# Kernel tuning notes

Measured on AMD Instinct MI355X. Metric: run time of the kernel, lower is better.

Reference implementation:

```python
import jax, jax.numpy as jnp
import numpy as np
import math

T, B, V, D = 8, 32, 50257, 256
N = 4096            # memory slots
H = 4               # attention heads
L = 2               # transformer layers
K = 3               # shift width
HALF = K // 2
WIN = 16            # controller window
RH, WH = 1, 1       # read / write heads
EPS = 1e-12


def _pe(win, d):
    pos = jnp.arange(win, dtype=jnp.float32)[:, None]
    div = jnp.exp(jnp.arange(0, d, 2, dtype=jnp.float32) * (-math.log(10000.0) / d))
    pe = jnp.zeros((win, d), dtype=jnp.float32)
    pe = pe.at[:, 0::2].set(jnp.sin(pos * div))
    pe = pe.at[:, 1::2].set(jnp.cos(pos * div))
    return pe[:, None, :]


def _ln(x, g, b, eps=1e-5):
    mu = x.mean(-1, keepdims=True)
    var = ((x - mu) ** 2).mean(-1, keepdims=True)
    return (x - mu) * jax.lax.rsqrt(var + eps) * g + b


def _mha(x, Wqkv, bqkv, Wo, bo):
    S, Bc, Dm = x.shape
    dh = Dm // H
    qkv = x @ Wqkv.T + bqkv
    q, k, v = jnp.split(qkv, 3, axis=-1)
    q = q.reshape(S, Bc, H, dh)
    k = k.reshape(S, Bc, H, dh)
    v = v.reshape(S, Bc, H, dh)
    logits = jnp.einsum('sbhd,tbhd->bhst', q, k) / math.sqrt(dh)
    a = jax.nn.softmax(logits, axis=-1)
    o = jnp.einsum('bhst,tbhd->sbhd', a, v).reshape(S, Bc, Dm)
    return o @ Wo.T + bo


def _addressing(key_v, beta, gate, shift, gamma, prev_w, memory):
    # key_v [B,M], beta/gate/gamma [B,1], shift [B,K], prev_w [B,N], memory [B,N,M]
    key_n = key_v / (jnp.linalg.norm(key_v, axis=-1, keepdims=True) + EPS)
    mem_n = memory / (jnp.linalg.norm(memory, axis=-1, keepdims=True) + EPS)
    cos = jnp.einsum('bnm,bm->bn', mem_n, key_n)
    wc = jax.nn.softmax(jax.nn.softplus(beta) * cos, axis=-1)
    g = jax.nn.sigmoid(gate)
    wg = g * wc + (1.0 - g) * prev_w
    s = jax.nn.softmax(shift, axis=-1)
    shifted = sum(s[:, k:k + 1] * jnp.roll(wg, k - HALF, axis=-1) for k in range(K))
    gp = 1.0 + jax.nn.softplus(gamma)
    wt = (shifted + EPS) ** gp
    return wt / (wt.sum(-1, keepdims=True) + EPS)


def setup_inputs() -> dict:
    key = jax.random.key(0)
    ks = iter(jax.random.split(key, 40))
    def w(shape, s=0.02):
        return jax.random.normal(next(ks), shape, jnp.float32) * s
    return {
        'tokens': jax.random.randint(next(ks), (T, B), 0, V, jnp.int32),
        'emb_W': w((V, D)),
        'read_gate_W': w((D, D)), 'read_gate_b': jnp.zeros((D,)),
        'film_W': w((2 * D, D)), 'film_b': jnp.zeros((2 * D,)),
        't_Wqkv': w((L, 3 * D, D)), 't_bqkv': jnp.zeros((L, 3 * D)),
        't_Wo': w((L, D, D)), 't_bo': jnp.zeros((L, D)),
        't_ln1_g': jnp.ones((L, D)), 't_ln1_b': jnp.zeros((L, D)),
        't_ln2_g': jnp.ones((L, D)), 't_ln2_b': jnp.zeros((L, D)),
        't_W1': w((L, 4 * D, D)), 't_b1': jnp.zeros((L, 4 * D)),
        't_W2': w((L, D, 4 * D)), 't_b2': jnp.zeros((L, D)),
        'out_ln_g': jnp.ones((D,)), 'out_ln_b': jnp.zeros((D,)),
        'lstm_Wih': w((2, 4 * D, D)), 'lstm_Whh': w((2, 4 * D, D)),
        'lstm_bih': jnp.zeros((2, 4 * D)), 'lstm_bhh': jnp.zeros((2, 4 * D)),
        'head_W': w((V, D)), 'head_b': jnp.zeros((V,)),
        'read_W': w((D + 3 + K, D)), 'read_b': jnp.zeros((D + 3 + K,)),
        'write_W': w((3 * D + 3 + K, D)), 'write_b': jnp.zeros((3 * D + 3 + K,)),
    }


def reference(tokens, emb_W, read_gate_W, read_gate_b, film_W, film_b,
              t_Wqkv, t_bqkv, t_Wo, t_bo, t_ln1_g, t_ln1_b, t_ln2_g, t_ln2_b,
              t_W1, t_b1, t_W2, t_b2, out_ln_g, out_ln_b,
              lstm_Wih, lstm_Whh, lstm_bih, lstm_bhh,
              head_W, head_b, read_W, read_b, write_W, write_b):
    pe = _pe(WIN, D)
    memory = jnp.zeros((B, N, D), jnp.float32)
    read_w = jnp.zeros((B, RH, N), jnp.float32).at[:, :, 0].set(1.0)
    write_w = jnp.zeros((B, WH, N), jnp.float32).at[:, :, 0].set(1.0)
    record = jnp.zeros((B, D), jnp.float32)
    hx = jnp.zeros((2, B, D), jnp.float32)
    cx = jnp.zeros((2, B, D), jnp.float32)
    hist = jnp.zeros((1, B, D), jnp.float32)
    logits_all = []
    for t in range(T):  # T fixed, sequential recurrence (context length grows)
        emb = emb_W[tokens[t]]                               # [B,D]
        r = jnp.einsum('bhn,bnm->bm', read_w, memory)        # sum over read heads
        fp = record @ film_W.T + film_b
        gam = 1.0 + jnp.tanh(fp[:, :D])
        bet = fp[:, D:]
        rg = jax.nn.sigmoid(record @ read_gate_W.T + read_gate_b)
        x_in = gam * emb + bet + rg * r
        ctx = jnp.concatenate([hist, x_in[None]], axis=0)
        if ctx.shape[0] > WIN:
            ctx = ctx[-WIN:]
        hist = ctx
        h = ctx + pe[:ctx.shape[0]]
        for l in range(L):  # norm_first pre-LN encoder layers (eval, relu FFN)
            h = h + _mha(_ln(h, t_ln1_g[l], t_ln1_b[l]), t_Wqkv[l], t_bqkv[l], t_Wo[l], t_bo[l])
            h = h + (jax.nn.relu(_ln(h, t_ln2_g[l], t_ln2_b[l]) @ t_W1[l].T + t_b1[l]) @ t_W2[l].T + t_b2[l])
        c_out = _ln(h[-1], out_ln_g, out_ln_b)
        # 2-layer LSTM single step (torch gate order i,f,g,o)
        x_l = c_out
        new_h, new_c = [], []
        for l in range(2):
            gates = x_l @ lstm_Wih[l].T + lstm_bih[l] + hx[l] @ lstm_Whh[l].T + lstm_bhh[l]
            i_g, f_g, g_g, o_g = jnp.split(gates, 4, axis=-1)
            c_new = jax.nn.sigmoid(f_g) * cx[l] + jax.nn.sigmoid(i_g) * jnp.tanh(g_g)
            h_new = jax.nn.sigmoid(o_g) * jnp.tanh(c_new)
            new_h.append(h_new); new_c.append(c_new)
            x_l = h_new
        hx = jnp.stack(new_h); cx = jnp.stack(new_c)
        record = hx[-1]
        c_out = c_out + x_l
        logits_all.append(c_out @ head_W.T + head_b)
        # read addressing
        rp = (c_out @ read_W.T + read_b).reshape(B, RH, -1)
        new_rw = []
        for hh in range(RH):
            p = rp[:, hh]
            new_rw.append(_addressing(p[:, :D], p[:, D:D + 1], p[:, D + 1:D + 2],
                                      p[:, D + 2:D + 2 + K], p[:, D + 2 + K:D + 3 + K],
                                      read_w[:, hh], memory))
        read_w = jnp.stack(new_rw, axis=1)
        # write addressing + erase/add (addressing uses pre-update memory)
        wp = (c_out @ write_W.T + write_b).reshape(B, WH, -1)
        mem_pre = memory
        new_ww = []
        for hh in range(WH):
            p = wp[:, hh]
            wt = _addressing(p[:, :D], p[:, D:D + 1], p[:, D + 1:D + 2],
                             p[:, D + 2:D + 2 + K], p[:, D + 2 + K:D + 3 + K],
                             write_w[:, hh], mem_pre)
            erase = jax.nn.sigmoid(p[:, D + 3 + K:2 * D + 3 + K])
            add = jnp.tanh(p[:, 2 * D + 3 + K:3 * D + 3 + K])
            memory = memory * (1.0 - wt[:, :, None] * erase[:, None, :]) + wt[:, :, None] * add[:, None, :]
            new_ww.append(wt)
        write_w = jnp.stack(new_ww, axis=1)
    return jnp.stack(logits_all, axis=0)  # [T, B, V]
```

## Files before the change

### kernel.cpp

```cpp
#include <hip/hip_runtime.h>
#include <math.h>

#define TT 8
#define BB 32
#define VV 50257
#define DD 256
#define NN 4096
#define EPS_ 1e-12f

typedef __attribute__((ext_vector_type(8))) short short8;
typedef __attribute__((ext_vector_type(4))) float f32x4;

__device__ __forceinline__ float sigf(float x) { return 1.f / (1.f + expf(-x)); }
__device__ __forceinline__ float softplusf_(float x) { return fmaxf(x, 0.f) + log1pf(expf(-fabsf(x))); }
__device__ __forceinline__ unsigned f2bf(float f) {
  union { float f; unsigned u; } c; c.f = f;
  return (c.u + 0x7FFFu + ((c.u >> 16) & 1u)) >> 16;
}
__device__ __forceinline__ float bf2f(unsigned u16) {
  union { unsigned u; float f; } c; c.u = u16 << 16; return c.f;
}

__device__ __forceinline__ float blk_sum(float v, float* s) {
#pragma unroll
  for (int o = 32; o > 0; o >>= 1) v += __shfl_down(v, o);
  __syncthreads();
  if ((threadIdx.x & 63) == 0) s[threadIdx.x >> 6] = v;
  __syncthreads();
  return s[0] + s[1] + s[2] + s[3];
}
__device__ __forceinline__ float blk_max(float v, float* s) {
#pragma unroll
  for (int o = 32; o > 0; o >>= 1) v = fmaxf(v, __shfl_down(v, o));
  __syncthreads();
  if ((threadIdx.x & 63) == 0) s[threadIdx.x >> 6] = v;
  __syncthreads();
  return fmaxf(fmaxf(s[0], s[1]), fmaxf(s[2], s[3]));
}

__global__ void init_k(float* rw, float* ww, float* hpe) {
  int i = blockIdx.x * 256 + threadIdx.x;
  if (i < BB) { rw[(size_t)i * NN] = 1.f; ww[(size_t)i * NN] = 1.f; }
  if (i < BB * DD) hpe[i] = (i & 1) ? 1.f : 0.f;
}

__global__ void cvtw_k(const float* __restrict__ W, unsigned short* __restrict__ Wh, int n4) {
  int i = blockIdx.x * 256 + threadIdx.x;
  if (i >= n4) return;
  float4 v = *(const float4*)(W + (size_t)i * 4);
  uint2 p;
  p.x = f2bf(v.x) | (f2bf(v.y) << 16);
  p.y = f2bf(v.z) | (f2bf(v.w) << 16);
  *(uint2*)(Wh + (size_t)i * 4) = p;
}

__global__ void catlstm_k(const float* __restrict__ Wih, const float* __restrict__ Whh,
                          const float* __restrict__ bih, const float* __restrict__ bhh,
                          unsigned short* __restrict__ Wc, float* __restrict__ cb) {
  int i = blockIdx.x * 256 + threadIdx.x;
  if (i >= 2 * 1024 * 512) return;
  int k = i & 511, np = (i >> 9) & 1023, l = i >> 19;
  int d = np >> 2, gate = np & 3;
  int src = gate * 256 + d;
  float v = (k < 256) ? Wih[((size_t)l * 1024 + src) * 256 + k]
                      : Whh[((size_t)l * 1024 + src) * 256 + (k - 256)];
  Wc[i] = (unsigned short)f2bf(v);
  if (k == 0) cb[l * 1024 + np] = bih[l * 1024 + src] + bhh[l * 1024 + src];
}

__global__ void catrw_k(const float* __restrict__ rW, const float* __restrict__ rb,
                        const float* __restrict__ wW, const float* __restrict__ wb,
                        unsigned short* __restrict__ Wrw, float* __restrict__ brw) {
  int i = blockIdx.x * 256 + threadIdx.x;
  if (i >= 1036 * 256) return;
  int k = i & 255, n = i >> 8;
  float v = (n < 262) ? rW[(size_t)n * 256 + k] : wW[(size_t)(n - 262) * 256 + k];
  Wrw[i] = (unsigned short)f2bf(v);
  if (k == 0) brw[n] = (n < 262) ? rb[n] : wb[n - 262];
}

__global__ void brc_k(const float* __restrict__ fb, const float* __restrict__ rb, float* __restrict__ brc) {
  int i = blockIdx.x * 256 + threadIdx.x;
  if (i < 512) brc[i] = fb[i];
  else if (i < 768) brc[i] = rb[i - 512];
}

__global__ __launch_bounds__(256) void ln0_k(const float* __restrict__ hpe,
                                             const float* __restrict__ g1, const float* __restrict__ b1,
                                             unsigned short* __restrict__ q1b) {
  __shared__ float s8[8];
  int b = blockIdx.x, d = threadIdx.x;
  float v = hpe[(size_t)b * 256 + d];
  float mu = blk_sum(v, s8) * (1.f / 256.f);
  float dd = v - mu;
  float var = blk_sum(dd * dd, s8) * (1.f / 256.f);
  float rs = rsqrtf(var + 1e-5f);
  q1b[(size_t)b * 256 + d] = (unsigned short)f2bf(dd * rs * g1[d] + b1[d]);
}

__device__ __forceinline__ void gA32f_dev(const unsigned short* __restrict__ A,
                                          const unsigned short* __restrict__ W,
                                          const float* __restrict__ bias,
                                          float* __restrict__ Cf, int ldc, int Nlim, int nblk) {
  const int tid = threadIdx.x, w = tid >> 6, l = tid & 63, r = l & 15, q = l >> 4;
  const int n = nblk * 64 + w * 16 + r;
  const unsigned short* Wp = W + (size_t)n * 256;
  f32x4 acc0 = {0.f, 0.f, 0.f, 0.f}, acc1 = {0.f, 0.f, 0.f, 0.f};
#pragma unroll
  for (int kt = 0; kt < 8; ++kt) {
    short8 a0 = *(const short8*)(A + r * 256 + kt * 32 + q * 8);
    short8 a1 = *(const short8*)(A + (16 + r) * 256 + kt * 32 + q * 8);
    short8 bf = *(const short8*)(Wp + kt * 32 + q * 8);
    acc0 = __builtin_amdgcn_mfma_f32_16x16x32_bf16(a0, bf, acc0, 0, 0, 0);
    acc1 = __builtin_amdgcn_mfma_f32_16x16x32_bf16(a1, bf, acc1, 0, 0, 0);
  }
  if (n >= Nlim) return;
  float bb = bias[n];
#pragma unroll
  for (int e = 0; e < 4; ++e) {
    int m1 = q * 4 + e, m2 = m1 + 16;
    Cf[(size_t)m1 * ldc + n] = acc0[e] + bb;
    Cf[(size_t)m2 * ldc + n] = acc1[e] + bb;
  }
}

__global__ __launch_bounds__(256) void gA_k(const unsigned short* __restrict__ A,
                                            const unsigned short* __restrict__ W,
                                            const float* __restrict__ bias,
                                            float* __restrict__ Cf, int ldc, int Nlim) {
  gA32f_dev(A + (size_t)blockIdx.y * 32 * 256, W, bias,
            Cf + (size_t)blockIdx.y * 32 * ldc, ldc, Nlim, blockIdx.x);
}

__global__ __launch_bounds__(256) void gAr_k(const unsigned short* __restrict__ A,
                                             const unsigned short* __restrict__ W,
                                             const float* __restrict__ bias,
                                             unsigned short* __restrict__ Cb, int ldc) {
  const int tid = threadIdx.x, w = tid >> 6, l = tid & 63, r = l & 15, q = l >> 4;
  const int n = blockIdx.x * 64 + w * 16 + r;
  const unsigned short* Ap = A + (size_t)blockIdx.y * 32 * 256;
  unsigned short* Cp = Cb + (size_t)blockIdx.y * 32 * ldc;
  const unsigned short* Wp = W + (size_t)n * 256;
  f32x4 acc0 = {0.f, 0.f, 0.f, 0.f}, acc1 = {0.f, 0.f, 0.f, 0.f};
#pragma unroll
  for (int kt = 0; kt < 8; ++kt) {
    short8 a0 = *(const short8*)(Ap + r * 256 + kt * 32 + q * 8);
    short8 a1 = *(const short8*)(Ap + (16 + r) * 256 + kt * 32 + q * 8);
    short8 bf = *(const short8*)(Wp + kt * 32 + q * 8);
    acc0 = __builtin_amdgcn_mfma_f32_16x16x32_bf16(a0, bf, acc0, 0, 0, 0);
    acc1 = __builtin_amdgcn_mfma_f32_16x16x32_bf16(a1, bf, acc1, 0, 0, 0);
  }
  float bb = bias[n];
#pragma unroll
  for (int e = 0; e < 4; ++e) {
    int m1 = q * 4 + e, m2 = m1 + 16;
    Cb[(size_t)(blockIdx.y * 32 + m1) * ldc + n] = (unsigned short)f2bf(fmaxf(acc0[e] + bb, 0.f));
    Cb[(size_t)(blockIdx.y * 32 + m2) * ldc + n] = (unsigned short)f2bf(fmaxf(acc1[e] + bb, 0.f));
  }
  (void)Cp;
}

template <int K>
__global__ __launch_bounds__(256) void gC_k(const unsigned short* __restrict__ A,
                                            const unsigned short* __restrict__ W,
                                            const float* __restrict__ bias,
                                            const float* __restrict__ resid,
                                            float* __restrict__ Hout) {
  const int tid = threadIdx.x, w = tid >> 6, l = tid & 63, r = l & 15, q = l >> 4;
  const int n = blockIdx.x * 64 + w * 16 + r;
  const int m0 = blockIdx.y * 32;
  const unsigned short* Ap = A + (size_t)m0 * K;
  const unsigned short* Wp = W + (size_t)n * K;
  f32x4 acc0 = {0.f, 0.f, 0.f, 0.f}, acc1 = {0.f, 0.f, 0.f, 0.f};
#pragma unroll 4
  for (int kt = 0; kt < K / 32; ++kt) {
    short8 a0 = *(const short8*)(Ap + (size_t)r * K + kt * 32 + q * 8);
    short8 a1 = *(const short8*)(Ap + (size_t)(16 + r) * K + kt * 32 + q * 8);
    short8 bf = *(const short8*)(Wp + kt * 32 + q * 8);
    acc0 = __builtin_amdgcn_mfma_f32_16x16x32_bf16(a0, bf, acc0, 0, 0, 0);
    acc1 = __builtin_amdgcn_mfma_f32_16x16x32_bf16(a1, bf, acc1, 0, 0, 0);
  }
  float bb = bias[n];
#pragma unroll
  for (int e = 0; e < 4; ++e) {
    int m1 = m0 + q * 4 + e, m2 = m1 + 16;
    Hout[(size_t)m1 * 256 + n] = acc0[e] + bb + resid[(size_t)m1 * 256 + n];
    Hout[(size_t)m2 * 256 + n] = acc1[e] + bb + resid[(size_t)m2 * 256 + n];
  }
}

__global__ __launch_bounds__(256) void addLN_k(const float* __restrict__ H,
                                               const float* __restrict__ g,
                                               const float* __restrict__ be,
                                               unsigned short* __restrict__ Xb, int xstride,
                                               float* __restrict__ c_out) {
  const int tid = threadIdx.x, w = tid >> 6, l = tid & 63;
  const int m0 = blockIdx.x * 32;
  const float4 g4 = *(const float4*)(g + l * 4);
  const float4 b4 = *(const float4*)(be + l * 4);
#pragma unroll
  for (int i = 0; i < 8; ++i) {
    int row = m0 + w * 8 + i;
    float4 v = *(const float4*)(H + (size_t)row * 256 + l * 4);
    float s1 = v.x + v.y + v.z + v.w;
    float s2 = v.x * v.x + v.y * v.y + v.z * v.z + v.w * v.w;
#pragma unroll
    for (int o = 32; o > 0; o >>= 1) { s1 += __shfl_xor(s1, o); s2 += __shfl_xor(s2, o); }
    float mu = s1 * (1.f / 256.f);
    float var = fmaxf(s2 * (1.f / 256.f) - mu * mu, 0.f);
    float rs = rsqrtf(var + 1e-5f);
    float y0 = (v.x - mu) * rs * g4.x + b4.x;
    float y1 = (v.y - mu) * rs * g4.y + b4.y;
    float y2 = (v.z - mu) * rs * g4.z + b4.z;
    float y3 = (v.w - mu) * rs * g4.w + b4.w;
    uint2 pk;
    pk.x = f2bf(y0) | (f2bf(y1) << 16);
    pk.y = f2bf(y2) | (f2bf(y3) << 16);
    *(uint2*)(Xb + (size_t)row * xstride + l * 4) = pk;
    if (c_out) {
      float4 cv = make_float4(y0, y1, y2, y3);
      *(float4*)(c_out + (size_t)row * 256 + l * 4) = cv;
    }
  }
}

__global__ __launch_bounds__(256) void auxg_k(const unsigned short* __restrict__ cfinb,
                                              const unsigned short* __restrict__ Wrw,
                                              const float* __restrict__ brw, float* __restrict__ rpwp,
                                              const unsigned short* __restrict__ record_b,
                                              const unsigned short* __restrict__ FRw,
                                              const float* __restrict__ brc, float* __restrict__ fp) {
  if (blockIdx.x < 17) gA32f_dev(cfinb, Wrw, brw, rpwp, 1036, 1036, blockIdx.x);
  else gA32f_dev(record_b, FRw, brc, fp, 768, 768, blockIdx.x - 17);
}

__global__ __launch_bounds__(128) void attn_k(const float* __restrict__ qkv,
                                              unsigned short* __restrict__ ao, int S) {
  int bh = blockIdx.x;
  int b = bh >> 2, h = bh & 3;
  __shared__ float q[9][64], k[9][64], v[9][64], lg[9][12];
  int tid = threadIdx.x;
  for (int i = tid; i < S * 64; i += 128) {
    int s = i >> 6, d = i & 63;
    const float* base = qkv + (size_t)(s * BB + b) * 768 + h * 64 + d;
    q[s][d] = base[0]; k[s][d] = base[256]; v[s][d] = base[512];
  }
  __syncthreads();
  for (int p = tid; p < S * S; p += 128) {
    int s = p / S, t2 = p % S;
    float acc = 0.f;
    for (int d = 0; d < 64; ++d) acc += q[s][d] * k[t2][d];
    lg[s][t2] = acc * 0.125f;
  }
  __syncthreads();
  if (tid < S) {
    float mx = -1e30f;
    for (int t2 = 0; t2 < S; ++t2) mx = fmaxf(mx, lg[tid][t2]);
    float sum = 0.f;
    for (int t2 = 0; t2 < S; ++t2) { float e = expf(lg[tid][t2] - mx); lg[tid][t2] = e; sum += e; }
    float inv = 1.f / sum;
    for (int t2 = 0; t2 < S; ++t2) lg[tid][t2] *= inv;
  }
  __syncthreads();
  for (int i = tid; i < S * 64; i += 128) {
    int s = i >> 6, d = i & 63;
    float o = 0.f;
    for (int t2 = 0; t2 < S; ++t2) o += lg[s][t2] * v[t2][d];
    ao[(size_t)(s * BB + b) * 256 + h * 64 + d] = (unsigned short)f2bf(o);
  }
}

__global__ __launch_bounds__(64) void attnl_k(const float* __restrict__ qkv,
                                              unsigned short* __restrict__ ao, int S) {
  int bh = blockIdx.x;
  int b = bh >> 2, h = bh & 3;
  int d = threadIdx.x;
  __shared__ float sc[9];
  float qd = qkv[(size_t)((S - 1) * BB + b) * 768 + h * 64 + d];
  for (int j = 0; j < S; ++j) {
    float p = qd * qkv[(size_t)(j * BB + b) * 768 + h * 64 + 256 + d];
#pragma unroll
    for (int o = 32; o > 0; o >>= 1) p += __shfl_down(p, o);
    if (d == 0) sc[j] = p * 0.125f;
  }
  __syncthreads();
  float mx = -1e30f;
  for (int j = 0; j < S; ++j) mx = fmaxf(mx, sc[j]);
  float pj[9], sum = 0.f;
  for (int j = 0; j < S; ++j) { pj[j] = expf(sc[j] - mx); sum += pj[j]; }
  float inv = 1.f / sum;
  float o = 0.f;
  for (int j = 0; j < S; ++j) o += pj[j] * inv * qkv[(size_t)(j * BB + b) * 768 + h * 64 + 512 + d];
  ao[(size_t)b * 256 + h * 64 + d] = (unsigned short)f2bf(o);
}

template <int LAST>
__global__ __launch_bounds__(256) void gL_k(const unsigned short* __restrict__ A,
                                            const unsigned short* __restrict__ W,
                                            const float* __restrict__ cbias,
                                            float* __restrict__ cx,
                                            unsigned short* __restrict__ li_own,
                                            unsigned short* __restrict__ li_next,
                                            const float* __restrict__ c_outp,
                                            unsigned short* __restrict__ cfinb,
                                            unsigned short* __restrict__ record_b) {
  __shared__ float g[32][68];
  const int tid = threadIdx.x, w = tid >> 6, l = tid & 63, r = l & 15, q = l >> 4;
  const int n = blockIdx.x * 64 + w * 16 + r;
  const unsigned short* Wp = W + (size_t)n * 512;
  f32x4 acc0 = {0.f, 0.f, 0.f, 0.f}, acc1 = {0.f, 0.f, 0.f, 0.f};
#pragma unroll 4
  for (int kt = 0; kt < 16; ++kt) {
    short8 a0 = *(const short8*)(A + (size_t)r * 512 + kt * 32 + q * 8);
    short8 a1 = *(const short8*)(A + (size_t)(16 + r) * 512 + kt * 32 + q * 8);
    short8 bf = *(const short8*)(Wp + kt * 32 + q * 8);
    acc0 = __builtin_amdgcn_mfma_f32_16x16x32_bf16(a0, bf, acc0, 0, 0, 0);
    acc1 = __builtin_amdgcn_mfma_f32_16x16x32_bf16(a1, bf, acc1, 0, 0, 0);
  }
  float bb = cbias[n];
  int nb = w * 16 + r;
#pragma unroll
  for (int e = 0; e < 4; ++e) {
    g[q * 4 + e][nb] = acc0[e] + bb;
    g[16 + q * 4 + e][nb] = acc1[e] + bb;
  }
  __syncthreads();
#pragma unroll
  for (int h2 = 0; h2 < 2; ++h2) {
    int u = tid + 256 * h2;
    int b = u >> 4, dd = u & 15;
    int dg = blockIdx.x * 16 + dd;
    float gi = g[b][dd * 4 + 0], gf = g[b][dd * 4 + 1];
    float gg = g[b][dd * 4 + 2], go = g[b][dd * 4 + 3];
    float c = sigf(gf) * cx[b * 256 + dg] + sigf(gi) * tanhf(gg);
    float hN = sigf(go) * tanhf(c);
    cx[b * 256 + dg] = c;
    li_own[(size_t)b * 512 + 256 + dg] = (unsigned short)f2bf(hN);
    if constexpr (LAST) {
      record_b[b * 256 + dg] = (unsigned short)f2bf(hN);
      cfinb[b * 256 + dg] = (unsigned short)f2bf(c_outp[b * 256 + dg] + hN);
    } else {
      li_next[(size_t)b * 512 + dg] = (unsigned short)f2bf(hN);
    }
  }
}

__global__ __launch_bounds__(256) void xinpw_k(const int* __restrict__ tokens,
                                               const float* __restrict__ embW,
                                               const float* __restrict__ fp,
                                               const float* __restrict__ rvec,
                                               const float* __restrict__ g1, const float* __restrict__ b1,
                                               float* __restrict__ hpe,
                                               unsigned short* __restrict__ q1b, int t) {
  __shared__ float s8[8];
  int b = blockIdx.x, d = threadIdx.x;
  float gam = 1.f + tanhf(fp[(size_t)b * 768 + d]);
  float bet = fp[(size_t)b * 768 + 256 + d];
  float rg = sigf(fp[(size_t)b * 768 + 512 + d]);
  int tok = tokens[t * BB + b];
  float emb = embW[(size_t)tok * 256 + d];
  float ang = (float)(t + 1) * expf(-logf(10000.f) * (float)(d & ~1) / 256.f);
  float pe = (d & 1) ? cosf(ang) : sinf(ang);
  float x = gam * emb + bet + rg * rvec[b * 256 + d] + pe;
  hpe[((size_t)(t + 1) * BB + b) * 256 + d] = x;
  float mu = blk_sum(x, s8) * (1.f / 256.f);
  float dd = x - mu;
  float var = blk_sum(dd * dd, s8) * (1.f / 256.f);
  float rs = rsqrtf(var + 1e-5f);
  q1b[((size_t)(t + 1) * BB + b) * 256 + d] = (unsigned short)f2bf(dd * rs * g1[d] + b1[d]);
}

__global__ __launch_bounds__(256) void fusePA_k(const unsigned short* __restrict__ Wh,
                                                const unsigned short* __restrict__ Ah,
                                                const float* __restrict__ hb,
                                                float* __restrict__ out,
                                                const unsigned short* __restrict__ mem,
                                                const float* __restrict__ rpwp,
                                                float* __restrict__ dr,
                                                float* __restrict__ dw,
                                                float* __restrict__ nrm) {
  __shared__ float kr[256], kw[256];
  const int bid = blockIdx.x;
  const int tid = threadIdx.x;
  if (bid < 786) {
    const int w = tid >> 6, l = tid & 63;
    const int r = l & 15, q = l >> 4;
    const int n = bid * 64 + w * 16 + r;
    const int nc = n < VV ? n : VV - 1;
    const short* Ap = (const short*)Ah;
    const short* Wp = (const short*)Wh + (size_t)nc * 256;
    short8 a0[8], a1[8], bf[8];
#pragma unroll
    for (int kt = 0; kt < 8; ++kt) {
      a0[kt] = *(const short8*)(Ap + r * 256 + kt * 32 + q * 8);
      a1[kt] = *(const short8*)(Ap + (16 + r) * 256 + kt * 32 + q * 8);
      bf[kt] = *(const short8*)(Wp + kt * 32 + q * 8);
    }
    f32x4 acc0 = {0.f, 0.f, 0.f, 0.f}, acc1 = {0.f, 0.f, 0.f, 0.f};
#pragma unroll
    for (int kt = 0; kt < 8; ++kt) {
      acc0 = __builtin_amdgcn_mfma_f32_16x16x32_bf16(a0[kt], bf[kt], acc0, 0, 0, 0);
      acc1 = __builtin_amdgcn_mfma_f32_16x16x32_bf16(a1[kt], bf[kt], acc1, 0, 0, 0);
    }
    if (n < VV) {
      float bb = hb[n];
#pragma unroll
      for (int e = 0; e < 4; ++e) {
        int m = q * 4 + e;
        out[(size_t)m * VV + n] = acc0[e] + bb;
        out[(size_t)(16 + m) * VV + n] = acc1[e] + bb;
      }
    }
    return;
  }
  const int idx = bid - 786;
  const int bx = idx & 255, by = idx >> 8;
  kr[tid] = rpwp[(size_t)by * 1036 + tid];
  kw[tid] = rpwp[(size_t)by * 1036 + 262 + tid];
  __syncthreads();
  int w = tid >> 6, lane = tid & 63;
  float4 kr4 = *(float4*)&kr[lane * 4];
  float4 kw4 = *(float4*)&kw[lane * 4];
  int n0 = bx * 16 + w * 4;
  for (int rr = 0; rr < 4; ++rr) {
    int n = n0 + rr;
    const unsigned short* row = mem + ((size_t)by * NN + n) * 256;
    uint2 pck = *(const uint2*)(row + lane * 4);
    float m0 = bf2f(pck.x & 0xffffu), m1 = bf2f(pck.x >> 16);
    float m2 = bf2f(pck.y & 0xffffu), m3 = bf2f(pck.y >> 16);
    float pr = m0 * kr4.x + m1 * kr4.y + m2 * kr4.z + m3 * kr4.w;
    float pw = m0 * kw4.x + m1 * kw4.y + m2 * kw4.z + m3 * kw4.w;
    float pn = m0 * m0 + m1 * m1 + m2 * m2 + m3 * m3;
#pragma unroll
    for (int o = 32; o > 0; o >>= 1) {
      pr += __shfl_down(pr, o); pw += __shfl_down(pw, o); pn += __shfl_down(pn, o);
    }
    if (lane == 0) {
      dr[(size_t)by * NN + n] = pr;
      dw[(size_t)by * NN + n] = pw;
      nrm[(size_t)by * NN + n] = pn;
    }
  }
}

__global__ __launch_bounds__(256) void addr_k(const float* __restrict__ dr,
                                              const float* __restrict__ dw,
                                              const float* __restrict__ nrm,
                                              const float* __restrict__ rpwp,
                                              float* rw, float* ww,
                                              float* __restrict__ ea,
                                              float* __restrict__ rvec) {
  __shared__ float wg[4096];
  __shared__ float s8[8];
  int head = blockIdx.x & 1, b = blockIdx.x >> 1;
  int tid = threadIdx.x;
  const float* p = rpwp + (size_t)b * 1036 + (head ? 262 : 0);
  const float* dot = (head ? dw : dr) + (size_t)b * NN;
  const float* n2 = nrm + (size_t)b * NN;
  float* wout = (head ? ww : rw) + (size_t)b * NN;

  float kv = p[tid];
  float kn = sqrtf(blk_sum(kv * kv, s8)) + EPS_;
  float beta = p[256], gate = p[257], sh0 = p[258], sh1 = p[259], sh2 = p[260], gamma = p[261];
  float spb = softplusf_(beta);
  float g = sigf(gate);
  float mx3 = fmaxf(sh0, fmaxf(sh1, sh2));
  float e0 = expf(sh0 - mx3), e1 = expf(sh1 - mx3), e2 = expf(sh2 - mx3);
  float esum = e0 + e1 + e2;
  float s0 = e0 / esum, s1 = e1 / esum, s2 = e2 / esum;
  float gp = 1.f + softplusf_(gamma);

  float l[16];
  float lmax = -1e30f;
#pragma unroll
  for (int i = 0; i < 16; ++i) {
    int n = tid + i * 256;
    float cs = dot[n] / ((sqrtf(n2[n]) + EPS_) * kn);
    l[i] = spb * cs;
    lmax = fmaxf(lmax, l[i]);
  }
  float Mx = blk_max(lmax, s8);
  float es = 0.f;
#pragma unroll
  for (int i = 0; i < 16; ++i) { l[i] = expf(l[i] - Mx); es += l[i]; }
  float SS = blk_sum(es, s8);
  float inv = 1.f / SS;
#pragma unroll
  for (int i = 0; i < 16; ++i) {
    int n = tid + i * 256;
    wg[n] = g * l[i] * inv + (1.f - g) * wout[n];
  }
  __syncthreads();
  float wt[16];
  float wsum = 0.f;
#pragma unroll
  for (int i = 0; i < 16; ++i) {
    int n = tid + i * 256;
    float sh = s0 * wg[(n + 1) & 4095] + s1 * wg[n] + s2 * wg[(n + 4095) & 4095];
    wt[i] = powf(sh + EPS_, gp);
    wsum += wt[i];
  }
  float WS = blk_sum(wsum, s8) + EPS_;
  float winv = 1.f / WS;
#pragma unroll
  for (int i = 0; i < 16; ++i) wout[tid + i * 256] = wt[i] * winv;

  if (head) {
    ea[(size_t)b * 512 + tid] = sigf(p[262 + tid]);
    ea[(size_t)b * 512 + 256 + tid] = tanhf(p[518 + tid]);
  } else {
    rvec[(size_t)b * 256 + tid] = 0.f;
  }
}

template <int FIRST>
__global__ __launch_bounds__(256) void passB_k(unsigned short* mem, const float* __restrict__ ww,
                                               const float* __restrict__ rw,
                                               const float* __restrict__ ea,
                                               float* __restrict__ rvec) {
  __shared__ float eS[256], aS[256];
  __shared__ float rred[4][256];
  int b = blockIdx.y, tid = threadIdx.x;
  eS[tid] = ea[(size_t)b * 512 + tid];
  aS[tid] = ea[(size_t)b * 512 + 256 + tid];
  __syncthreads();
  int w = tid >> 6, lane = tid & 63;
  float4 e4 = *(float4*)&eS[lane * 4];
  float4 a4 = *(float4*)&aS[lane * 4];
  float4 racc = make_float4(0.f, 0.f, 0.f, 0.f);
  int n0 = blockIdx.x * 128 + w * 32;
  for (int rr = 0; rr < 32; ++rr) {
    int n = n0 + rr;
    float wt = ww[(size_t)b * NN + n];
    float rwv = rw[(size_t)b * NN + n];
    unsigned short* row = mem + ((size_t)b * NN + n) * 256;
    float m0, m1, m2, m3;
    if (FIRST) {
      m0 = wt * a4.x; m1 = wt * a4.y; m2 = wt * a4.z; m3 = wt * a4.w;
    } else {
      uint2 p = *(const uint2*)(row + lane * 4);
      m0 = bf2f(p.x & 0xffffu) * (1.f - wt * e4.x) + wt * a4.x;
      m1 = bf2f(p.x >> 16) * (1.f - wt * e4.y) + wt * a4.y;
      m2 = bf2f(p.y & 0xffffu) * (1.f - wt * e4.z) + wt * a4.z;
      m3 = bf2f(p.y >> 16) * (1.f - wt * e4.w) + wt * a4.w;
    }
    uint2 pk;
    pk.x = f2bf(m0) | (f2bf(m1) << 16);
    pk.y = f2bf(m2) | (f2bf(m3) << 16);
    *(uint2*)(row + lane * 4) = pk;
    racc.x += rwv * m0; racc.y += rwv * m1; racc.z += rwv * m2; racc.w += rwv * m3;
  }
  rred[w][lane * 4 + 0] = racc.x;
  rred[w][lane * 4 + 1] = racc.y;
  rred[w][lane * 4 + 2] = racc.z;
  rred[w][lane * 4 + 3] = racc.w;
  __syncthreads();
  float s = rred[0][tid] + rred[1][tid] + rred[2][tid] + rred[3][tid];
  atomicAdd(rvec + (size_t)b * 256 + tid, s);
}

extern "C" void kernel_launch(void* const* d_in, const int* in_sizes, int n_in,
                              void* d_out, int out_size, void* d_ws, size_t ws_size,
                              hipStream_t stream) {
  const int* tokens = (const int*)d_in[0];
  const float* emb_W = (const float*)d_in[1];
  const float* read_gate_W = (const float*)d_in[2];
  const float* read_gate_b = (const float*)d_in[3];
  const float* film_W = (const float*)d_in[4];
  const float* film_b = (const float*)d_in[5];
  const float* t_Wqkv = (const float*)d_in[6];
  const float* t_bqkv = (const float*)d_in[7];
  const float* t_Wo = (const float*)d_in[8];
  const float* t_bo = (const float*)d_in[9];
  const float* t_ln1_g = (const float*)d_in[10];
  const float* t_ln1_b = (const float*)d_in[11];
  const float* t_ln2_g = (const float*)d_in[12];
  const float* t_ln2_b = (const float*)d_in[13];
  const float* t_W1 = (const float*)d_in[14];
  const float* t_b1 = (const float*)d_in[15];
  const float* t_W2 = (const float*)d_in[16];
  const float* t_b2 = (const float*)d_in[17];
  const float* out_ln_g = (const float*)d_in[18];
  const float* out_ln_b = (const float*)d_in[19];
  const float* lstm_Wih = (const float*)d_in[20];
  const float* lstm_Whh = (const float*)d_in[21];
  const float* lstm_bih = (const float*)d_in[22];
  const float* lstm_bhh = (const float*)d_in[23];
  const float* head_W = (const float*)d_in[24];
  const float* head_b = (const float*)d_in[25];
  const float* read_W = (const float*)d_in[26];
  const float* read_b = (const float*)d_in[27];
  const float* write_W = (const float*)d_in[28];
  const float* write_b = (const float*)d_in[29];
  float* out = (float*)d_out;

  float* ws = (float*)d_ws;
  size_t off = 0;
  float* read_w = ws + off; off += (size_t)BB * NN;
  float* write_w = ws + off; off += (size_t)BB * NN;
  float* cx = ws + off; off += 2 * BB * DD;
  float* r_vec = ws + off; off += BB * DD;
  float* dot_r = ws + off; off += (size_t)BB * NN;
  float* dot_w = ws + off; off += (size_t)BB * NN;
  float* norm2 = ws + off; off += (size_t)BB * NN;
  unsigned short* record_b = (unsigned short*)(ws + off); off += BB * DD / 2;
  unsigned short* lstm_in_b = (unsigned short*)(ws + off); off += 2 * BB * 512 / 2;
  size_t zero_floats = off;
  unsigned short* memory = (unsigned short*)(ws + off); off += (size_t)BB * NN * DD / 2;
  float* hpe = ws + off; off += 9 * BB * DD;
  float* h = ws + off; off += 9 * BB * DD;
  float* h2 = ws + off; off += BB * DD;
  float* qkvC = ws + off; off += 9 * BB * 768;
  float* qkv2 = ws + off; off += 9 * BB * 768;
  float* fp = ws + off; off += BB * 768;
  float* c_out = ws + off; off += BB * DD;
  float* rpwp = ws + off; off += BB * 1036;
  float* ea = ws + off; off += BB * 2 * DD;
  unsigned short* q1b = (unsigned short*)(ws + off); off += 9 * BB * DD / 2;
  unsigned short* q2b = (unsigned short*)(ws + off); off += 9 * BB * DD / 2;
  unsigned short* x2b = (unsigned short*)(ws + off); off += 9 * BB * DD / 2;
  unsigned short* x2b2 = (unsigned short*)(ws + off); off += BB * DD / 2;
  unsigned short* ao1_b = (unsigned short*)(ws + off); off += 9 * BB * DD / 2;
  unsigned short* ao2_b = (unsigned short*)(ws + off); off += BB * DD / 2;
  unsigned short* mid_b = (unsigned short*)(ws + off); off += 9 * BB * 1024 / 2;
  unsigned short* cfinb = (unsigned short*)(ws + off); off += BB * DD / 2;
  unsigned short* Wh = (unsigned short*)(ws + off); off += (size_t)VV * 256 / 2;
  unsigned short* Wq_b = (unsigned short*)(ws + off); off += 2 * 768 * 256 / 2;
  unsigned short* Wo_b = (unsigned short*)(ws + off); off += 2 * 256 * 256 / 2;
  unsigned short* W1_b = (unsigned short*)(ws + off); off += 2 * 1024 * 256 / 2;
  unsigned short* W2_b = (unsigned short*)(ws + off); off += 2 * 256 * 1024 / 2;
  unsigned short* Wc_b = (unsigned short*)(ws + off); off += 2 * 1024 * 512 / 2;
  unsigned short* Wrw_b = (unsigned short*)(ws + off); off += 1088 * 256 / 2;
  unsigned short* FR_b = (unsigned short*)(ws + off); off += 768 * 256 / 2;
  float* cb2 = ws + off; off += 2 * 1024;
  float* brw = ws + off; off += 1040;
  float* brc = ws + off; off += 768;
  if (ws_size < off * sizeof(float)) return;

  (void)hipMemsetAsync(ws, 0, zero_floats * sizeof(float), stream);
  (void)hipMemsetAsync(Wrw_b + (size_t)1036 * 256, 0, (size_t)52 * 256 * 2, stream);
  init_k<<<32, 256, 0, stream>>>(read_w, write_w, hpe);
  cvtw_k<<<(VV * 256 / 4 + 255) / 256, 256, 0, stream>>>(head_W, Wh, VV * 256 / 4);
  cvtw_k<<<(2 * 768 * 256 / 4 + 255) / 256, 256, 0, stream>>>(t_Wqkv, Wq_b, 2 * 768 * 256 / 4);
  cvtw_k<<<(2 * 256 * 256 / 4 + 255) / 256, 256, 0, stream>>>(t_Wo, Wo_b, 2 * 256 * 256 / 4);
  cvtw_k<<<(2 * 1024 * 256 / 4 + 255) / 256, 256, 0, stream>>>(t_W1, W1_b, 2 * 1024 * 256 / 4);
  cvtw_k<<<(2 * 256 * 1024 / 4 + 255) / 256, 256, 0, stream>>>(t_W2, W2_b, 2 * 256 * 1024 / 4);
  cvtw_k<<<(512 * 256 / 4 + 255) / 256, 256, 0, stream>>>(film_W, FR_b, 512 * 256 / 4);
  cvtw_k<<<(256 * 256 / 4 + 255) / 256, 256, 0, stream>>>(read_gate_W, FR_b + 512 * 256, 256 * 256 / 4);
  catlstm_k<<<4096, 256, 0, stream>>>(lstm_Wih, lstm_Whh, lstm_bih, lstm_bhh, Wc_b, cb2);
  catrw_k<<<1036, 256, 0, stream>>>(read_W, read_b, write_W, write_b, Wrw_b, brw);
  brc_k<<<3, 256, 0, stream>>>(film_b, read_gate_b, brc);
  ln0_k<<<BB, 256, 0, stream>>>(hpe, t_ln1_g, t_ln1_b, q1b);
  gA_k<<<dim3(12, 1), 256, 0, stream>>>(q1b, Wq_b, t_bqkv, qkvC, 768, 768);
  gA_k<<<dim3(12, 1), 256, 0, stream>>>(record_b, FR_b, brc, fp, 768, 768);

  for (int t = 0; t < TT; ++t) {
    const int S = t + 2;

    xinpw_k<<<BB, 256, 0, stream>>>(tokens, emb_W, fp, r_vec, t_ln1_g, t_ln1_b, hpe, q1b, t);
    gA_k<<<dim3(12, 1), 256, 0, stream>>>(q1b + (size_t)(t + 1) * BB * 256, Wq_b, t_bqkv,
                                          qkvC + (size_t)(t + 1) * BB * 768, 768, 768);
    attn_k<<<BB * 4, 128, 0, stream>>>(qkvC, ao1_b, S);
    gC_k<256><<<dim3(4, S), 256, 0, stream>>>(ao1_b, Wo_b, t_bo, hpe, h);
    addLN_k<<<S, 256, 0, stream>>>(h, t_ln2_g, t_ln2_b, x2b, 256, nullptr);
    gAr_k<<<dim3(16, S), 256, 0, stream>>>(x2b, W1_b, t_b1, mid_b, 1024);
    gC_k<1024><<<dim3(4, S), 256, 0, stream>>>(mid_b, W2_b, t_b2, h, h);
    addLN_k<<<S, 256, 0, stream>>>(h, t_ln1_g + 256, t_ln1_b + 256, q2b, 256, nullptr);
    gA_k<<<dim3(12, S), 256, 0, stream>>>(q2b, Wq_b + 768 * 256, t_bqkv + 768, qkv2, 768, 768);
    attnl_k<<<BB * 4, 64, 0, stream>>>(qkv2, ao2_b, S);
    gC_k<256><<<dim3(4, 1), 256, 0, stream>>>(ao2_b, Wo_b + 256 * 256, t_bo + 256,
                                              h + (size_t)(S - 1) * BB * 256, h2);
    addLN_k<<<1, 256, 0, stream>>>(h2, t_ln2_g + 256, t_ln2_b + 256, x2b2, 256, nullptr);
    gAr_k<<<dim3(16, 1), 256, 0, stream>>>(x2b2, W1_b + 1024 * 256, t_b1 + 1024, mid_b, 1024);
    gC_k<1024><<<dim3(4, 1), 256, 0, stream>>>(mid_b, W2_b + 256 * 1024, t_b2 + 256, h2, h2);
    addLN_k<<<1, 256, 0, stream>>>(h2, out_ln_g, out_ln_b, lstm_in_b, 512, c_out);
    gL_k<0><<<16, 256, 0, stream>>>(lstm_in_b, Wc_b, cb2, cx, lstm_in_b, lstm_in_b + BB * 512,
                                    nullptr, nullptr, nullptr);
    gL_k<1><<<16, 256, 0, stream>>>(lstm_in_b + BB * 512, Wc_b + (size_t)1024 * 512, cb2 + 1024,
                                    cx + BB * DD, lstm_in_b + BB * 512, nullptr, c_out, cfinb, record_b);
    if (t < TT - 1) {
      auxg_k<<<29, 256, 0, stream>>>(cfinb, Wrw_b, brw, rpwp, record_b, FR_b, brc, fp);
      if (t > 0)
        fusePA_k<<<786 + 8192, 256, 0, stream>>>(Wh, cfinb, head_b, out + (size_t)t * BB * VV,
                                                 memory, rpwp, dot_r, dot_w, norm2);
      else
        fusePA_k<<<786, 256, 0, stream>>>(Wh, cfinb, head_b, out + (size_t)t * BB * VV,
                                          memory, rpwp, dot_r, dot_w, norm2);
      addr_k<<<2 * BB, 256, 0, stream>>>(dot_r, dot_w, norm2, rpwp, read_w, write_w, ea, r_vec);
      if (t == 0)
        passB_k<1><<<dim3(NN / 128, BB), 256, 0, stream>>>(memory, write_w, read_w, ea, r_vec);
      else
        passB_k<0><<<dim3(NN / 128, BB), 256, 0, stream>>>(memory, write_w, read_w, ea, r_vec);
    } else {
      fusePA_k<<<786, 256, 0, stream>>>(Wh, cfinb, head_b, out + (size_t)t * BB * VV,
                                        memory, rpwp, dot_r, dot_w, norm2);
    }
  }
}
```

Baseline: 1.481 ms.

## Compute memory key dot products with bf16 MFMA using hi/lo split keys

The memory-scan part of fusePA_k now computes the read and write key dot products with 16x16x32 bf16 MFMA. Each fp32 key is split into a bf16 high and low part so the result stays close to fp32 precision, and the two halves are summed with a lane shuffle. Each block now covers 128 memory rows instead of 16, which cuts the extra grid from 8192 blocks to 1024 and removes the per-row wave shuffle reductions. The squared norms are accumulated in scalar code from the same loaded fragments. The costs are that 12 of the 16 MFMA columns are wasted padding and the keys lose a little precision through the bf16 split.

After: 1.403 ms (median of 2 runs). 1.06x faster.

```diff
diff --git a/kernel.cpp b/kernel.cpp
--- a/kernel.cpp
+++ b/kernel.cpp
@@ -139,7 +139,6 @@
   const int tid = threadIdx.x, w = tid >> 6, l = tid & 63, r = l & 15, q = l >> 4;
   const int n = blockIdx.x * 64 + w * 16 + r;
   const unsigned short* Ap = A + (size_t)blockIdx.y * 32 * 256;
-  unsigned short* Cp = Cb + (size_t)blockIdx.y * 32 * ldc;
   const unsigned short* Wp = W + (size_t)n * 256;
   f32x4 acc0 = {0.f, 0.f, 0.f, 0.f}, acc1 = {0.f, 0.f, 0.f, 0.f};
 #pragma unroll
@@ -157,7 +156,6 @@
     Cb[(size_t)(blockIdx.y * 32 + m1) * ldc + n] = (unsigned short)f2bf(fmaxf(acc0[e] + bb, 0.f));
     Cb[(size_t)(blockIdx.y * 32 + m2) * ldc + n] = (unsigned short)f2bf(fmaxf(acc1[e] + bb, 0.f));
   }
-  (void)Cp;
 }
 
 template <int K>
@@ -379,7 +377,7 @@
                                                 float* __restrict__ dr,
                                                 float* __restrict__ dw,
                                                 float* __restrict__ nrm) {
-  __shared__ float kr[256], kw[256];
+  __shared__ unsigned short kS[4][256];
   const int bid = blockIdx.x;
   const int tid = threadIdx.x;
   if (bid < 786) {
@@ -414,31 +412,60 @@
     return;
   }
   const int idx = bid - 786;
-  const int bx = idx & 255, by = idx >> 8;
-  kr[tid] = rpwp[(size_t)by * 1036 + tid];
-  kw[tid] = rpwp[(size_t)by * 1036 + 262 + tid];
-  __syncthreads();
-  int w = tid >> 6, lane = tid & 63;
-  float4 kr4 = *(float4*)&kr[lane * 4];
-  float4 kw4 = *(float4*)&kw[lane * 4];
-  int n0 = bx * 16 + w * 4;
-  for (int rr = 0; rr < 4; ++rr) {
-    int n = n0 + rr;
-    const unsigned short* row = mem + ((size_t)by * NN + n) * 256;
-    uint2 pck = *(const uint2*)(row + lane * 4);
-    float m0 = bf2f(pck.x & 0xffffu), m1 = bf2f(pck.x >> 16);
-    float m2 = bf2f(pck.y & 0xffffu), m3 = bf2f(pck.y >> 16);
-    float pr = m0 * kr4.x + m1 * kr4.y + m2 * kr4.z + m3 * kr4.w;
-    float pw = m0 * kw4.x + m1 * kw4.y + m2 * kw4.z + m3 * kw4.w;
-    float pn = m0 * m0 + m1 * m1 + m2 * m2 + m3 * m3;
-#pragma unroll
-    for (int o = 32; o > 0; o >>= 1) {
-      pr += __shfl_down(pr, o); pw += __shfl_down(pw, o); pn += __shfl_down(pn, o);
-    }
-    if (lane == 0) {
-      dr[(size_t)by * NN + n] = pr;
-      dw[(size_t)by * NN + n] = pw;
-      nrm[(size_t)by * NN + n] = pn;
+  const int bx = idx & 31, by = idx >> 5;
+  {
+    float kr = rpwp[(size_t)by * 1036 + tid];
+    float kw = rpwp[(size_t)by * 1036 + 262 + tid];
+    unsigned krh = f2bf(kr), kwh = f2bf(kw);
+    kS[0][tid] = (unsigned short)krh;
+    kS[1][tid] = (unsigned short)kwh;
+    kS[2][tid] = (unsigned short)f2bf(kr - bf2f(krh));
+    kS[3][tid] = (unsigned short)f2bf(kw - bf2f(kwh));
+  }
+  __syncthreads();
+  const int w = tid >> 6, l = tid & 63, col = l & 15, ko = (l >> 4) * 8;
+  short8 bfrag[8];
+#pragma unroll
+  for (int kt = 0; kt < 8; ++kt) {
+    if (col < 4) bfrag[kt] = *(const short8*)(&kS[col][kt * 32 + ko]);
+    else bfrag[kt] = short8{0, 0, 0, 0, 0, 0, 0, 0};
+  }
+  const int base = bx * 128 + w * 32;
+  const unsigned short* Ap0 = mem + ((size_t)by * NN + base + col) * 256 + ko;
+  const unsigned short* Ap1 = mem + ((size_t)by * NN + base + 16 + col) * 256 + ko;
+  f32x4 acc0 = {0.f, 0.f, 0.f, 0.f}, acc1 = {0.f, 0.f, 0.f, 0.f};
+  float pn0 = 0.f, pn1 = 0.f;
+#pragma unroll
+  for (int kt = 0; kt < 8; ++kt) {
+    short8 a0 = *(const short8*)(Ap0 + kt * 32);
+    short8 a1 = *(const short8*)(Ap1 + kt * 32);
+    acc0 = __builtin_amdgcn_mfma_f32_16x16x32_bf16(a0, bfrag[kt], acc0, 0, 0, 0);
+    acc1 = __builtin_amdgcn_mfma_f32_16x16x32_bf16(a1, bfrag[kt], acc1, 0, 0, 0);
+#pragma unroll
+    for (int j = 0; j < 8; ++j) {
+      float v0 = bf2f((unsigned short)a0[j]);
+      float v1 = bf2f((unsigned short)a1[j]);
+      pn0 += v0 * v0;
+      pn1 += v1 * v1;
+    }
+  }
+  pn0 += __shfl_xor(pn0, 16); pn0 += __shfl_xor(pn0, 32);
+  pn1 += __shfl_xor(pn1, 16); pn1 += __shfl_xor(pn1, 32);
+  if (l < 16) {
+    nrm[(size_t)by * NN + base + l] = pn0;
+    nrm[(size_t)by * NN + base + 16 + l] = pn1;
+  }
+#pragma unroll
+  for (int e = 0; e < 4; ++e) {
+    float s0 = acc0[e] + __shfl_xor(acc0[e], 2);
+    float s1 = acc1[e] + __shfl_xor(acc1[e], 2);
+    int row = (l >> 4) * 4 + e;
+    if (col == 0) {
+      dr[(size_t)by * NN + base + row] = s0;
+      dr[(size_t)by * NN + base + 16 + row] = s1;
+    } else if (col == 1) {
+      dw[(size_t)by * NN + base + row] = s0;
+      dw[(size_t)by * NN + base + 16 + row] = s1;
     }
   }
 }
@@ -681,7 +708,7 @@
     if (t < TT - 1) {
       auxg_k<<<29, 256, 0, stream>>>(cfinb, Wrw_b, brw, rpwp, record_b, FR_b, brc, fp);
       if (t > 0)
-        fusePA_k<<<786 + 8192, 256, 0, stream>>>(Wh, cfinb, head_b, out + (size_t)t * BB * VV,
+        fusePA_k<<<786 + 1024, 256, 0, stream>>>(Wh, cfinb, head_b, out + (size_t)t * BB * VV,
                                                  memory, rpwp, dot_r, dot_w, norm2);
       else
         fusePA_k<<<786, 256, 0, stream>>>(Wh, cfinb, head_b, out + (size_t)t * BB * VV,
```
